# Optimization experiments

Measured on AMD Instinct MI355X. Metric: run time of the kernel, lower is better.

The kernel has to match this reference:

```python
import jax, jax.numpy as jnp
import numpy as np

NUM_EXPERTS = 8
TOP_K = 2
HIDDEN = 1024
INTER = 4096
STD = 0.02


def setup_inputs() -> dict:
    key = jax.random.key(0)
    k0, k1, k2, k3 = jax.random.split(key, 4)
    hidden_states = jax.random.normal(k0, (2, 2048, HIDDEN), dtype=jnp.float32)
    gate_w = jax.random.normal(k1, (NUM_EXPERTS, HIDDEN), dtype=jnp.float32) * (HIDDEN ** -0.5)
    w1 = jax.random.normal(k2, (NUM_EXPERTS, INTER, HIDDEN), dtype=jnp.float32) * STD  # c_fc.weight
    w2 = jax.random.normal(k3, (NUM_EXPERTS, HIDDEN, INTER), dtype=jnp.float32) * STD  # c_proj.weight
    return {"hidden_states": hidden_states, "gate_w": gate_w, "w1": w1, "w2": w2}


def reference(hidden_states, gate_w, w1, w2):
    B, S, H = hidden_states.shape
    x = hidden_states.reshape(-1, H)                      # [T, H]
    T = x.shape[0]
    # ---- routing ----
    router_logits = x @ gate_w.T                          # [T, E]
    top_vals, top_idx = jax.lax.top_k(router_logits, TOP_K)
    router_weights = jax.nn.softmax(top_vals.astype(jnp.float32), axis=-1).astype(x.dtype)
    # dense combine matrix with exactly top_k nonzeros per row (math-equivalent
    # to the sort/grouped-GEMM/scatter-combine pipeline in the torch module)
    combine = jnp.zeros((T, NUM_EXPERTS), x.dtype).at[
        jnp.arange(T)[:, None], top_idx
    ].set(router_weights)                                 # [T, E]
    # ---- experts ----
    h = jax.nn.gelu(jnp.einsum('th,eih->eti', x, w1), approximate=False)  # [E, T, I]
    y = jnp.einsum('eti,ehi->eth', h, w2)                 # [E, T, H]
    out = jnp.einsum('eth,te->th', y, combine)            # weighted combine
    return out.reshape(B, S, H), router_logits
```

## Files before the change

### kernel.cpp

```cpp
#include <hip/hip_runtime.h>

#define T 4096
#define Hdim 1024
#define Idim 4096
#define NE 8
#define OUT0 4194304
#define SPLITK 2
#define BK 64

#define SLOT_CAP 9216

#define W1B_OFF 0u
#define W2B_OFF 67108864u
#define XB_OFF  134217728u
#define HB_OFF  142606336u
#define YB_OFF  218103808u
#define META_OFF 255852544u
#define M_COUNTS 0
#define M_CURS   8
#define M_OFFS   16
#define M_TEXP   32
#define M_TSLOT  8224
#define M_STOK   16416
#define M_TWF    25632

typedef short bf16x8 __attribute__((ext_vector_type(8)));
typedef float f32x4  __attribute__((ext_vector_type(4)));

__device__ __forceinline__ unsigned short f2bf(float f) {
    unsigned int b = __float_as_uint(f);
    b += 0x7fffu + ((b >> 16) & 1u);
    return (unsigned short)(b >> 16);
}
__device__ __forceinline__ float bf2f(unsigned short s) {
    return __uint_as_float(((unsigned int)s) << 16);
}

__global__ void zero_k(int* meta) {
    int i = blockIdx.x * blockDim.x + threadIdx.x;
    if (i < 16) meta[i] = 0;
    if (i < SLOT_CAP) meta[M_STOK + i] = -1;
}

__global__ void cvt_w_k(const float* __restrict__ w1, const float* __restrict__ w2,
                        unsigned short* __restrict__ w1b, unsigned short* __restrict__ w2b,
                        int n4each) {
    int i = blockIdx.x * blockDim.x + threadIdx.x;
    const float4* src; ushort4* dst; int j;
    if (i < n4each) { src = (const float4*)w1; dst = (ushort4*)w1b; j = i; }
    else            { src = (const float4*)w2; dst = (ushort4*)w2b; j = i - n4each; }
    float4 v = src[j];
    ushort4 o;
    o.x = f2bf(v.x); o.y = f2bf(v.y); o.z = f2bf(v.z); o.w = f2bf(v.w);
    dst[j] = o;
}

__global__ void router_k(const float* __restrict__ x, const float* __restrict__ gw,
                         float* __restrict__ logits_out, int* __restrict__ texp,
                         float* __restrict__ twf, int* __restrict__ counts,
                         unsigned short* __restrict__ xb) {
    int wv = threadIdx.x >> 6, lane = threadIdx.x & 63;
    int t = blockIdx.x * 4 + wv;
    const float* xp = x + (size_t)t * Hdim;
    unsigned short* xbp = xb + (size_t)t * Hdim;
    float s[NE];
    #pragma unroll
    for (int e = 0; e < NE; e++) s[e] = 0.f;
    #pragma unroll
    for (int j = 0; j < 16; j++) {
        float xv = xp[lane + 64 * j];
        xbp[lane + 64 * j] = f2bf(xv);
        #pragma unroll
        for (int e = 0; e < NE; e++) s[e] += xv * gw[e * Hdim + lane + 64 * j];
    }
    #pragma unroll
    for (int e = 0; e < NE; e++) {
        #pragma unroll
        for (int off = 32; off > 0; off >>= 1) s[e] += __shfl_xor(s[e], off);
    }
    if (lane == 0) {
        #pragma unroll
        for (int e = 0; e < NE; e++) logits_out[t * NE + e] = s[e];
        int i0 = 0; float v0 = s[0];
        #pragma unroll
        for (int e = 1; e < NE; e++) if (s[e] > v0) { v0 = s[e]; i0 = e; }
        int i1 = -1; float v1 = -3.4e38f;
        #pragma unroll
        for (int e = 0; e < NE; e++) if (e != i0 && s[e] > v1) { v1 = s[e]; i1 = e; }
        float e1 = expf(v1 - v0);
        float inv = 1.f / (1.f + e1);
        texp[2 * t] = i0; texp[2 * t + 1] = i1;
        twf[2 * t] = inv; twf[2 * t + 1] = e1 * inv;
        atomicAdd(&counts[i0], 1);
        atomicAdd(&counts[i1], 1);
    }
}

__global__ void offsets_k(const int* __restrict__ counts, int* __restrict__ offs) {
    if (threadIdx.x == 0 && blockIdx.x == 0) {
        int a = 0; offs[0] = 0;
        for (int e = 0; e < NE; e++) { a += (counts[e] + 127) & ~127; offs[e + 1] = a; }
    }
}

__global__ void assign_k(const int* __restrict__ texp, const int* __restrict__ offs,
                         int* __restrict__ curs, int* __restrict__ stok, int* __restrict__ tslot) {
    int p = blockIdx.x * blockDim.x + threadIdx.x;
    int e = texp[p];
    int slot = offs[e] + atomicAdd(&curs[e], 1);
    stok[slot] = p >> 1;
    tslot[p] = slot;
}

#define PF_LOAD(base_off) \
    pa0 = *(const uint4*)(gA0 + (base_off)); pa1 = *(const uint4*)(gA1 + (base_off)); \
    pa2 = *(const uint4*)(gA2 + (base_off)); pa3 = *(const uint4*)(gA3 + (base_off)); \
    pb0 = *(const uint4*)(gB0 + (base_off)); pb1 = *(const uint4*)(gB1 + (base_off)); \
    pb2 = *(const uint4*)(gB2 + (base_off)); pb3 = *(const uint4*)(gB3 + (base_off));
#define PF_STORE() \
    *(uint4*)la0 = pa0; *(uint4*)la1 = pa1; *(uint4*)la2 = pa2; *(uint4*)la3 = pa3; \
    *(uint4*)lb0 = pb0; *(uint4*)lb1 = pb1; *(uint4*)lb2 = pb2; *(uint4*)lb3 = pb3;

__global__ __launch_bounds__(256, 2) void gemm1_k(
    const unsigned short* __restrict__ xb, const unsigned short* __restrict__ w1b,
    const int* __restrict__ offs, const int* __restrict__ stok,
    unsigned short* __restrict__ hb) {
    __shared__ __align__(16) unsigned short As[128 * BK];
    __shared__ __align__(16) unsigned short Bs[128 * BK];
    const int rt = blockIdx.y, ct = blockIdx.x;
    const int row0 = rt * 128;
    if (row0 >= offs[NE]) return;
    int e = 0;
    #pragma unroll
    for (int q = 1; q < NE; q++) if (offs[q] <= row0) e = q;

    const int tid = threadIdx.x;
    const int lane = tid & 63, wv = tid >> 6;
    const int srow = lane >> 3;
    const int schunk = (lane & 7) ^ srow;

    int r0 = wv * 32 + 0 * 8 + srow, r1 = wv * 32 + 1 * 8 + srow;
    int r2 = wv * 32 + 2 * 8 + srow, r3 = wv * 32 + 3 * 8 + srow;
    int t0 = stok[row0 + r0]; if (t0 < 0) t0 = 0;
    int t1 = stok[row0 + r1]; if (t1 < 0) t1 = 0;
    int t2 = stok[row0 + r2]; if (t2 < 0) t2 = 0;
    int t3 = stok[row0 + r3]; if (t3 < 0) t3 = 0;
    const unsigned short* gA0 = xb + (size_t)t0 * Hdim + schunk * 8;
    const unsigned short* gA1 = xb + (size_t)t1 * Hdim + schunk * 8;
    const unsigned short* gA2 = xb + (size_t)t2 * Hdim + schunk * 8;
    const unsigned short* gA3 = xb + (size_t)t3 * Hdim + schunk * 8;
    const unsigned short* gB0 = w1b + ((size_t)e * Idim + ct * 128 + r0) * Hdim + schunk * 8;
    const unsigned short* gB1 = w1b + ((size_t)e * Idim + ct * 128 + r1) * Hdim + schunk * 8;
    const unsigned short* gB2 = w1b + ((size_t)e * Idim + ct * 128 + r2) * Hdim + schunk * 8;
    const unsigned short* gB3 = w1b + ((size_t)e * Idim + ct * 128 + r3) * Hdim + schunk * 8;
    unsigned short* la0 = As + (wv * 32 + 0 * 8) * BK + lane * 8;
    unsigned short* la1 = As + (wv * 32 + 1 * 8) * BK + lane * 8;
    unsigned short* la2 = As + (wv * 32 + 2 * 8) * BK + lane * 8;
    unsigned short* la3 = As + (wv * 32 + 3 * 8) * BK + lane * 8;
    unsigned short* lb0 = Bs + (wv * 32 + 0 * 8) * BK + lane * 8;
    unsigned short* lb1 = Bs + (wv * 32 + 1 * 8) * BK + lane * 8;
    unsigned short* lb2 = Bs + (wv * 32 + 2 * 8) * BK + lane * 8;
    unsigned short* lb3 = Bs + (wv * 32 + 3 * 8) * BK + lane * 8;

    f32x4 acc[4][4] = {};
    const int mrow = (wv & 1) * 64, ncol = (wv >> 1) * 64;
    const int fr = lane & 15, qd = lane >> 4;

    uint4 pa0, pa1, pa2, pa3, pb0, pb1, pb2, pb3;
    PF_LOAD(0)
    PF_STORE()
    __syncthreads();

    const int NIT = Hdim / BK;
    for (int it = 0; it < NIT; it++) {
        if (it + 1 < NIT) { PF_LOAD((it + 1) * BK) }
        #pragma unroll
        for (int ko = 0; ko < 2; ko++) {
            bf16x8 af[4], bff[4];
            #pragma unroll
            for (int mi = 0; mi < 4; mi++)
                af[mi]  = *(const bf16x8*)&As[(mrow + mi * 16 + fr) * BK + ((((ko << 2) | qd) ^ (fr & 7)) << 3)];
            #pragma unroll
            for (int ni = 0; ni < 4; ni++)
                bff[ni] = *(const bf16x8*)&Bs[(ncol + ni * 16 + fr) * BK + ((((ko << 2) | qd) ^ (fr & 7)) << 3)];
            #pragma unroll
            for (int mi = 0; mi < 4; mi++)
                #pragma unroll
                for (int ni = 0; ni < 4; ni++)
                    acc[mi][ni] = __builtin_amdgcn_mfma_f32_16x16x32_bf16(af[mi], bff[ni], acc[mi][ni], 0, 0, 0);
        }
        if (it + 1 < NIT) {
            __syncthreads();
            PF_STORE()
            __syncthreads();
        }
    }
    #pragma unroll
    for (int mi = 0; mi < 4; mi++) {
        #pragma unroll
        for (int ni = 0; ni < 4; ni++) {
            #pragma unroll
            for (int r = 0; r < 4; r++) {
                int row = row0 + mrow + mi * 16 + qd * 4 + r;
                int col = ct * 128 + ncol + ni * 16 + fr;
                float v = acc[mi][ni][r];
                float u = v * (1.f + 0.044715f * v * v);
                float g = v / (1.f + __expf(-1.5957691216f * u));
                hb[(size_t)row * Idim + col] = f2bf(g);
            }
        }
    }
}

__global__ __launch_bounds__(256, 2) void gemm2_k(
    const unsigned short* __restrict__ hb, const unsigned short* __restrict__ w2b,
    const int* __restrict__ offs, unsigned short* __restrict__ y16) {
    __shared__ __align__(16) unsigned short As[128 * BK];
    __shared__ __align__(16) unsigned short Bs[128 * BK];
    const int id = blockIdx.x;
    const int k8 = id & 7;
    const int j  = id >> 3;
    const int ct = j & 7;
    const int j8 = j >> 3;
    const int rtL = j8 % 9, kz = j8 / 9;
    const int rt = k8 * 9 + rtL;
    const int row0 = rt * 128;
    if (row0 >= offs[NE]) return;
    int e = 0;
    #pragma unroll
    for (int q = 1; q < NE; q++) if (offs[q] <= row0) e = q;

    const int tid = threadIdx.x;
    const int lane = tid & 63, wv = tid >> 6;
    const int srow = lane >> 3;
    const int schunk = (lane & 7) ^ srow;

    int r0 = wv * 32 + 0 * 8 + srow, r1 = wv * 32 + 1 * 8 + srow;
    int r2 = wv * 32 + 2 * 8 + srow, r3 = wv * 32 + 3 * 8 + srow;
    const unsigned short* gA0 = hb + (size_t)(row0 + r0) * Idim + schunk * 8;
    const unsigned short* gA1 = hb + (size_t)(row0 + r1) * Idim + schunk * 8;
    const unsigned short* gA2 = hb + (size_t)(row0 + r2) * Idim + schunk * 8;
    const unsigned short* gA3 = hb + (size_t)(row0 + r3) * Idim + schunk * 8;
    const unsigned short* gB0 = w2b + ((size_t)e * Hdim + ct * 128 + r0) * Idim + schunk * 8;
    const unsigned short* gB1 = w2b + ((size_t)e * Hdim + ct * 128 + r1) * Idim + schunk * 8;
    const unsigned short* gB2 = w2b + ((size_t)e * Hdim + ct * 128 + r2) * Idim + schunk * 8;
    const unsigned short* gB3 = w2b + ((size_t)e * Hdim + ct * 128 + r3) * Idim + schunk * 8;
    unsigned short* la0 = As + (wv * 32 + 0 * 8) * BK + lane * 8;
    unsigned short* la1 = As + (wv * 32 + 1 * 8) * BK + lane * 8;
    unsigned short* la2 = As + (wv * 32 + 2 * 8) * BK + lane * 8;
    unsigned short* la3 = As + (wv * 32 + 3 * 8) * BK + lane * 8;
    unsigned short* lb0 = Bs + (wv * 32 + 0 * 8) * BK + lane * 8;
    unsigned short* lb1 = Bs + (wv * 32 + 1 * 8) * BK + lane * 8;
    unsigned short* lb2 = Bs + (wv * 32 + 2 * 8) * BK + lane * 8;
    unsigned short* lb3 = Bs + (wv * 32 + 3 * 8) * BK + lane * 8;

    f32x4 acc[4][4] = {};
    const int mrow = (wv & 1) * 64, ncol = (wv >> 1) * 64;
    const int fr = lane & 15, qd = lane >> 4;

    const int k0 = kz * (Idim / SPLITK);
    uint4 pa0, pa1, pa2, pa3, pb0, pb1, pb2, pb3;
    PF_LOAD(k0)
    PF_STORE()
    __syncthreads();

    const int NIT = (Idim / SPLITK) / BK;
    for (int it = 0; it < NIT; it++) {
        if (it + 1 < NIT) { PF_LOAD(k0 + (it + 1) * BK) }
        #pragma unroll
        for (int ko = 0; ko < 2; ko++) {
            bf16x8 af[4], bff[4];
            #pragma unroll
            for (int mi = 0; mi < 4; mi++)
                af[mi]  = *(const bf16x8*)&As[(mrow + mi * 16 + fr) * BK + ((((ko << 2) | qd) ^ (fr & 7)) << 3)];
            #pragma unroll
            for (int ni = 0; ni < 4; ni++)
                bff[ni] = *(const bf16x8*)&Bs[(ncol + ni * 16 + fr) * BK + ((((ko << 2) | qd) ^ (fr & 7)) << 3)];
            #pragma unroll
            for (int mi = 0; mi < 4; mi++)
                #pragma unroll
                for (int ni = 0; ni < 4; ni++)
                    acc[mi][ni] = __builtin_amdgcn_mfma_f32_16x16x32_bf16(af[mi], bff[ni], acc[mi][ni], 0, 0, 0);
        }
        if (it + 1 < NIT) {
            __syncthreads();
            PF_STORE()
            __syncthreads();
        }
    }
    unsigned short* yk = y16 + (size_t)kz * SLOT_CAP * Hdim;
    #pragma unroll
    for (int mi = 0; mi < 4; mi++) {
        #pragma unroll
        for (int ni = 0; ni < 4; ni++) {
            #pragma unroll
            for (int r = 0; r < 4; r++) {
                int row = row0 + mrow + mi * 16 + qd * 4 + r;
                int col = ct * 128 + ncol + ni * 16 + fr;
                yk[(size_t)row * Hdim + col] = f2bf(acc[mi][ni][r]);
            }
        }
    }
}

__global__ void combine_k(const unsigned short* __restrict__ y16, const int* __restrict__ tslot,
                          const float* __restrict__ twf, float* __restrict__ out) {
    int i = blockIdx.x * blockDim.x + threadIdx.x;
    int t = i >> 7, rem = i & 127;
    int s0 = tslot[2 * t], s1 = tslot[2 * t + 1];
    float w0 = twf[2 * t], w1 = twf[2 * t + 1];
    const uint4* y0 = (const uint4*)(y16);
    const uint4* y1 = (const uint4*)(y16 + (size_t)SLOT_CAP * Hdim);
    uint4 a0 = y0[(size_t)s0 * 128 + rem];
    uint4 a1 = y1[(size_t)s0 * 128 + rem];
    uint4 b0 = y0[(size_t)s1 * 128 + rem];
    uint4 b1 = y1[(size_t)s1 * 128 + rem];
    float o[8];
    #pragma unroll
    for (int j = 0; j < 4; j++) {
        unsigned int ua0 = ((const unsigned int*)&a0)[j], ua1 = ((const unsigned int*)&a1)[j];
        unsigned int ub0 = ((const unsigned int*)&b0)[j], ub1 = ((const unsigned int*)&b1)[j];
        float alo = bf2f((unsigned short)ua0) + bf2f((unsigned short)ua1);
        float ahi = bf2f((unsigned short)(ua0 >> 16)) + bf2f((unsigned short)(ua1 >> 16));
        float blo = bf2f((unsigned short)ub0) + bf2f((unsigned short)ub1);
        float bhi = bf2f((unsigned short)(ub0 >> 16)) + bf2f((unsigned short)(ub1 >> 16));
        o[2 * j]     = w0 * alo + w1 * blo;
        o[2 * j + 1] = w0 * ahi + w1 * bhi;
    }
    float4* out4 = (float4*)out;
    out4[2 * i]     = make_float4(o[0], o[1], o[2], o[3]);
    out4[2 * i + 1] = make_float4(o[4], o[5], o[6], o[7]);
}

extern "C" void kernel_launch(void* const* d_in, const int* in_sizes, int n_in,
                              void* d_out, int out_size, void* d_ws, size_t ws_size,
                              hipStream_t stream) {
    const float* x  = (const float*)d_in[0];
    const float* gw = (const float*)d_in[1];
    const float* w1 = (const float*)d_in[2];
    const float* w2 = (const float*)d_in[3];
    float* out = (float*)d_out;

    char* ws = (char*)d_ws;
    unsigned short* w1b = (unsigned short*)(ws + W1B_OFF);
    unsigned short* w2b = (unsigned short*)(ws + W2B_OFF);
    unsigned short* xb  = (unsigned short*)(ws + XB_OFF);
    unsigned short* hb  = (unsigned short*)(ws + HB_OFF);
    unsigned short* y16 = (unsigned short*)(ws + YB_OFF);
    int*            meta = (int*)(ws + META_OFF);
    int* counts = meta + M_COUNTS;
    int* curs   = meta + M_CURS;
    int* offs   = meta + M_OFFS;
    int* texp   = meta + M_TEXP;
    int* tslot  = meta + M_TSLOT;
    int* stok   = meta + M_STOK;
    float* twf  = (float*)(meta + M_TWF);

    zero_k<<<36, 256, 0, stream>>>(meta);
    cvt_w_k<<<65536, 256, 0, stream>>>(w1, w2, w1b, w2b, NE * Idim * Hdim / 4);
    router_k<<<T / 4, 256, 0, stream>>>(x, gw, out + OUT0, texp, twf, counts, xb);
    offsets_k<<<1, 64, 0, stream>>>(counts, offs);
    assign_k<<<32, 256, 0, stream>>>(texp, offs, curs, stok, tslot);
    gemm1_k<<<dim3(Idim / 128, SLOT_CAP / 128), 256, 0, stream>>>(xb, w1b, offs, stok, hb);
    gemm2_k<<<(Hdim / 128) * (SLOT_CAP / 128) * SPLITK, 256, 0, stream>>>(hb, w2b, offs, y16);
    combine_k<<<T * Hdim / 8 / 256, 256, 0, stream>>>(y16, tslot, twf, out);
}
```

Measured before the change: 636.2 us.

## Use direct global-to-LDS loads in expert GEMMs and fold small setup kernels

Both expert GEMMs now stage A/B tiles with global_load_lds, copying straight into shared memory instead of through registers. This drops the register prefetch buffers and raises the occupancy hint to 3 blocks per CU. The zero and offsets kernels are removed: zeroing moves into the weight conversion kernel, and each consumer recomputes the per-expert offsets from counts. The trade-off is that the single-buffered loop no longer overlaps the next tile's load with MFMA compute, so each iteration waits on the load before computing.

```diff
diff --git a/kernel.cpp b/kernel.cpp
--- a/kernel.cpp
+++ b/kernel.cpp
@@ -36,16 +36,17 @@
     return __uint_as_float(((unsigned int)s) << 16);
 }
 
-__global__ void zero_k(int* meta) {
-    int i = blockIdx.x * blockDim.x + threadIdx.x;
-    if (i < 16) meta[i] = 0;
-    if (i < SLOT_CAP) meta[M_STOK + i] = -1;
-}
+#define GLD(gsrc, ldst) \
+    __builtin_amdgcn_global_load_lds( \
+        (const __attribute__((address_space(1))) unsigned int*)(gsrc), \
+        (__attribute__((address_space(3))) unsigned int*)(ldst), 16, 0, 0)
 
 __global__ void cvt_w_k(const float* __restrict__ w1, const float* __restrict__ w2,
                         unsigned short* __restrict__ w1b, unsigned short* __restrict__ w2b,
-                        int n4each) {
+                        int n4each, int* __restrict__ meta) {
     int i = blockIdx.x * blockDim.x + threadIdx.x;
+    if (i < 16) meta[M_COUNTS + i] = 0;
+    if (i < SLOT_CAP) meta[M_STOK + i] = -1;
     const float4* src; ushort4* dst; int j;
     if (i < n4each) { src = (const float4*)w1; dst = (ushort4*)w1b; j = i; }
     else            { src = (const float4*)w2; dst = (ushort4*)w2b; j = i - n4each; }
@@ -96,39 +97,33 @@
     }
 }
 
-__global__ void offsets_k(const int* __restrict__ counts, int* __restrict__ offs) {
-    if (threadIdx.x == 0 && blockIdx.x == 0) {
-        int a = 0; offs[0] = 0;
-        for (int e = 0; e < NE; e++) { a += (counts[e] + 127) & ~127; offs[e + 1] = a; }
-    }
-}
-
-__global__ void assign_k(const int* __restrict__ texp, const int* __restrict__ offs,
+__global__ void assign_k(const int* __restrict__ texp, const int* __restrict__ counts,
                          int* __restrict__ curs, int* __restrict__ stok, int* __restrict__ tslot) {
     int p = blockIdx.x * blockDim.x + threadIdx.x;
     int e = texp[p];
-    int slot = offs[e] + atomicAdd(&curs[e], 1);
+    int off = 0;
+    #pragma unroll
+    for (int q = 0; q < NE; q++) {
+        int pc = (counts[q] + 127) & ~127;
+        off += (q < e) ? pc : 0;
+    }
+    int slot = off + atomicAdd(&curs[e], 1);
     stok[slot] = p >> 1;
     tslot[p] = slot;
 }
 
-#define PF_LOAD(base_off) \
-    pa0 = *(const uint4*)(gA0 + (base_off)); pa1 = *(const uint4*)(gA1 + (base_off)); \
-    pa2 = *(const uint4*)(gA2 + (base_off)); pa3 = *(const uint4*)(gA3 + (base_off)); \
-    pb0 = *(const uint4*)(gB0 + (base_off)); pb1 = *(const uint4*)(gB1 + (base_off)); \
-    pb2 = *(const uint4*)(gB2 + (base_off)); pb3 = *(const uint4*)(gB3 + (base_off));
-#define PF_STORE() \
-    *(uint4*)la0 = pa0; *(uint4*)la1 = pa1; *(uint4*)la2 = pa2; *(uint4*)la3 = pa3; \
-    *(uint4*)lb0 = pb0; *(uint4*)lb1 = pb1; *(uint4*)lb2 = pb2; *(uint4*)lb3 = pb3;
-
-__global__ __launch_bounds__(256, 2) void gemm1_k(
+__global__ __launch_bounds__(256, 3) void gemm1_k(
     const unsigned short* __restrict__ xb, const unsigned short* __restrict__ w1b,
-    const int* __restrict__ offs, const int* __restrict__ stok,
+    const int* __restrict__ counts, const int* __restrict__ stok,
     unsigned short* __restrict__ hb) {
     __shared__ __align__(16) unsigned short As[128 * BK];
     __shared__ __align__(16) unsigned short Bs[128 * BK];
     const int rt = blockIdx.y, ct = blockIdx.x;
     const int row0 = rt * 128;
+    int offs[NE + 1];
+    offs[0] = 0;
+    #pragma unroll
+    for (int q = 0; q < NE; q++) offs[q + 1] = offs[q] + ((counts[q] + 127) & ~127);
     if (row0 >= offs[NE]) return;
     int e = 0;
     #pragma unroll
@@ -139,41 +134,32 @@
     const int srow = lane >> 3;
     const int schunk = (lane & 7) ^ srow;
 
-    int r0 = wv * 32 + 0 * 8 + srow, r1 = wv * 32 + 1 * 8 + srow;
-    int r2 = wv * 32 + 2 * 8 + srow, r3 = wv * 32 + 3 * 8 + srow;
-    int t0 = stok[row0 + r0]; if (t0 < 0) t0 = 0;
-    int t1 = stok[row0 + r1]; if (t1 < 0) t1 = 0;
-    int t2 = stok[row0 + r2]; if (t2 < 0) t2 = 0;
-    int t3 = stok[row0 + r3]; if (t3 < 0) t3 = 0;
-    const unsigned short* gA0 = xb + (size_t)t0 * Hdim + schunk * 8;
-    const unsigned short* gA1 = xb + (size_t)t1 * Hdim + schunk * 8;
-    const unsigned short* gA2 = xb + (size_t)t2 * Hdim + schunk * 8;
-    const unsigned short* gA3 = xb + (size_t)t3 * Hdim + schunk * 8;
-    const unsigned short* gB0 = w1b + ((size_t)e * Idim + ct * 128 + r0) * Hdim + schunk * 8;
-    const unsigned short* gB1 = w1b + ((size_t)e * Idim + ct * 128 + r1) * Hdim + schunk * 8;
-    const unsigned short* gB2 = w1b + ((size_t)e * Idim + ct * 128 + r2) * Hdim + schunk * 8;
-    const unsigned short* gB3 = w1b + ((size_t)e * Idim + ct * 128 + r3) * Hdim + schunk * 8;
-    unsigned short* la0 = As + (wv * 32 + 0 * 8) * BK + lane * 8;
-    unsigned short* la1 = As + (wv * 32 + 1 * 8) * BK + lane * 8;
-    unsigned short* la2 = As + (wv * 32 + 2 * 8) * BK + lane * 8;
-    unsigned short* la3 = As + (wv * 32 + 3 * 8) * BK + lane * 8;
-    unsigned short* lb0 = Bs + (wv * 32 + 0 * 8) * BK + lane * 8;
-    unsigned short* lb1 = Bs + (wv * 32 + 1 * 8) * BK + lane * 8;
-    unsigned short* lb2 = Bs + (wv * 32 + 2 * 8) * BK + lane * 8;
-    unsigned short* lb3 = Bs + (wv * 32 + 3 * 8) * BK + lane * 8;
+    const unsigned short* gA[4];
+    const unsigned short* gB[4];
+    unsigned short* lA[4];
+    unsigned short* lB[4];
+    #pragma unroll
+    for (int g = 0; g < 4; g++) {
+        int r = wv * 32 + g * 8 + srow;
+        int t = stok[row0 + r]; if (t < 0) t = 0;
+        gA[g] = xb + (size_t)t * Hdim + schunk * 8;
+        gB[g] = w1b + ((size_t)e * Idim + ct * 128 + r) * Hdim + schunk * 8;
+        lA[g] = As + (wv * 32 + g * 8) * BK;
+        lB[g] = Bs + (wv * 32 + g * 8) * BK;
+    }
 
     f32x4 acc[4][4] = {};
     const int mrow = (wv & 1) * 64, ncol = (wv >> 1) * 64;
     const int fr = lane & 15, qd = lane >> 4;
 
-    uint4 pa0, pa1, pa2, pa3, pb0, pb1, pb2, pb3;
-    PF_LOAD(0)
-    PF_STORE()
-    __syncthreads();
-
     const int NIT = Hdim / BK;
     for (int it = 0; it < NIT; it++) {
-        if (it + 1 < NIT) { PF_LOAD((it + 1) * BK) }
+        #pragma unroll
+        for (int g = 0; g < 4; g++) {
+            GLD(gA[g] + it * BK, lA[g]);
+            GLD(gB[g] + it * BK, lB[g]);
+        }
+        __syncthreads();
         #pragma unroll
         for (int ko = 0; ko < 2; ko++) {
             bf16x8 af[4], bff[4];
@@ -189,11 +175,7 @@
                 for (int ni = 0; ni < 4; ni++)
                     acc[mi][ni] = __builtin_amdgcn_mfma_f32_16x16x32_bf16(af[mi], bff[ni], acc[mi][ni], 0, 0, 0);
         }
-        if (it + 1 < NIT) {
-            __syncthreads();
-            PF_STORE()
-            __syncthreads();
-        }
+        __syncthreads();
     }
     #pragma unroll
     for (int mi = 0; mi < 4; mi++) {
@@ -212,9 +194,9 @@
     }
 }
 
-__global__ __launch_bounds__(256, 2) void gemm2_k(
+__global__ __launch_bounds__(256, 3) void gemm2_k(
     const unsigned short* __restrict__ hb, const unsigned short* __restrict__ w2b,
-    const int* __restrict__ offs, unsigned short* __restrict__ y16) {
+    const int* __restrict__ counts, unsigned short* __restrict__ y16) {
     __shared__ __align__(16) unsigned short As[128 * BK];
     __shared__ __align__(16) unsigned short Bs[128 * BK];
     const int id = blockIdx.x;
@@ -225,6 +207,10 @@
     const int rtL = j8 % 9, kz = j8 / 9;
     const int rt = k8 * 9 + rtL;
     const int row0 = rt * 128;
+    int offs[NE + 1];
+    offs[0] = 0;
+    #pragma unroll
+    for (int q = 0; q < NE; q++) offs[q + 1] = offs[q] + ((counts[q] + 127) & ~127);
     if (row0 >= offs[NE]) return;
     int e = 0;
     #pragma unroll
@@ -235,38 +221,32 @@
     const int srow = lane >> 3;
     const int schunk = (lane & 7) ^ srow;
 
-    int r0 = wv * 32 + 0 * 8 + srow, r1 = wv * 32 + 1 * 8 + srow;
-    int r2 = wv * 32 + 2 * 8 + srow, r3 = wv * 32 + 3 * 8 + srow;
-    const unsigned short* gA0 = hb + (size_t)(row0 + r0) * Idim + schunk * 8;
-    const unsigned short* gA1 = hb + (size_t)(row0 + r1) * Idim + schunk * 8;
-    const unsigned short* gA2 = hb + (size_t)(row0 + r2) * Idim + schunk * 8;
-    const unsigned short* gA3 = hb + (size_t)(row0 + r3) * Idim + schunk * 8;
-    const unsigned short* gB0 = w2b + ((size_t)e * Hdim + ct * 128 + r0) * Idim + schunk * 8;
-    const unsigned short* gB1 = w2b + ((size_t)e * Hdim + ct * 128 + r1) * Idim + schunk * 8;
-    const unsigned short* gB2 = w2b + ((size_t)e * Hdim + ct * 128 + r2) * Idim + schunk * 8;
-    const unsigned short* gB3 = w2b + ((size_t)e * Hdim + ct * 128 + r3) * Idim + schunk * 8;
-    unsigned short* la0 = As + (wv * 32 + 0 * 8) * BK + lane * 8;
-    unsigned short* la1 = As + (wv * 32 + 1 * 8) * BK + lane * 8;
-    unsigned short* la2 = As + (wv * 32 + 2 * 8) * BK + lane * 8;
-    unsigned short* la3 = As + (wv * 32 + 3 * 8) * BK + lane * 8;
-    unsigned short* lb0 = Bs + (wv * 32 + 0 * 8) * BK + lane * 8;
-    unsigned short* lb1 = Bs + (wv * 32 + 1 * 8) * BK + lane * 8;
-    unsigned short* lb2 = Bs + (wv * 32 + 2 * 8) * BK + lane * 8;
-    unsigned short* lb3 = Bs + (wv * 32 + 3 * 8) * BK + lane * 8;
+    const unsigned short* gA[4];
+    const unsigned short* gB[4];
+    unsigned short* lA[4];
+    unsigned short* lB[4];
+    #pragma unroll
+    for (int g = 0; g < 4; g++) {
+        int r = wv * 32 + g * 8 + srow;
+        gA[g] = hb + (size_t)(row0 + r) * Idim + schunk * 8;
+        gB[g] = w2b + ((size_t)e * Hdim + ct * 128 + r) * Idim + schunk * 8;
+        lA[g] = As + (wv * 32 + g * 8) * BK;
+        lB[g] = Bs + (wv * 32 + g * 8) * BK;
+    }
 
     f32x4 acc[4][4] = {};
     const int mrow = (wv & 1) * 64, ncol = (wv >> 1) * 64;
     const int fr = lane & 15, qd = lane >> 4;
 
     const int k0 = kz * (Idim / SPLITK);
-    uint4 pa0, pa1, pa2, pa3, pb0, pb1, pb2, pb3;
-    PF_LOAD(k0)
-    PF_STORE()
-    __syncthreads();
-
     const int NIT = (Idim / SPLITK) / BK;
     for (int it = 0; it < NIT; it++) {
-        if (it + 1 < NIT) { PF_LOAD(k0 + (it + 1) * BK) }
+        #pragma unroll
+        for (int g = 0; g < 4; g++) {
+            GLD(gA[g] + k0 + it * BK, lA[g]);
+            GLD(gB[g] + k0 + it * BK, lB[g]);
+        }
+        __syncthreads();
         #pragma unroll
         for (int ko = 0; ko < 2; ko++) {
             bf16x8 af[4], bff[4];
@@ -282,11 +262,7 @@
                 for (int ni = 0; ni < 4; ni++)
                     acc[mi][ni] = __builtin_amdgcn_mfma_f32_16x16x32_bf16(af[mi], bff[ni], acc[mi][ni], 0, 0, 0);
         }
-        if (it + 1 < NIT) {
-            __syncthreads();
-            PF_STORE()
-            __syncthreads();
-        }
+        __syncthreads();
     }
     unsigned short* yk = y16 + (size_t)kz * SLOT_CAP * Hdim;
     #pragma unroll
@@ -350,18 +326,15 @@
     int*            meta = (int*)(ws + META_OFF);
     int* counts = meta + M_COUNTS;
     int* curs   = meta + M_CURS;
-    int* offs   = meta + M_OFFS;
     int* texp   = meta + M_TEXP;
     int* tslot  = meta + M_TSLOT;
     int* stok   = meta + M_STOK;
     float* twf  = (float*)(meta + M_TWF);
 
-    zero_k<<<36, 256, 0, stream>>>(meta);
-    cvt_w_k<<<65536, 256, 0, stream>>>(w1, w2, w1b, w2b, NE * Idim * Hdim / 4);
+    cvt_w_k<<<65536, 256, 0, stream>>>(w1, w2, w1b, w2b, NE * Idim * Hdim / 4, meta);
     router_k<<<T / 4, 256, 0, stream>>>(x, gw, out + OUT0, texp, twf, counts, xb);
-    offsets_k<<<1, 64, 0, stream>>>(counts, offs);
-    assign_k<<<32, 256, 0, stream>>>(texp, offs, curs, stok, tslot);
-    gemm1_k<<<dim3(Idim / 128, SLOT_CAP / 128), 256, 0, stream>>>(xb, w1b, offs, stok, hb);
-    gemm2_k<<<(Hdim / 128) * (SLOT_CAP / 128) * SPLITK, 256, 0, stream>>>(hb, w2b, offs, y16);
+    assign_k<<<32, 256, 0, stream>>>(texp, counts, curs, stok, tslot);
+    gemm1_k<<<dim3(Idim / 128, SLOT_CAP / 128), 256, 0, stream>>>(xb, w1b, counts, stok, hb);
+    gemm2_k<<<(Hdim / 128) * (SLOT_CAP / 128) * SPLITK, 256, 0, stream>>>(hb, w2b, counts, y16);
     combine_k<<<T * Hdim / 8 / 256, 256, 0, stream>>>(y16, tslot, twf, out);
 }
```

Result: faster. 618.1 us (-2.8%).
